# Performance work log

Hardware: AMD Instinct MI355X
Metric: run time of the kernel (lower is better)

## Reference

```python
import jax, jax.numpy as jnp
import numpy as np

HEADS = 8
DIM_HEAD = 64
SCALE = DIM_HEAD ** -0.5
EPS = 1e-7


def setup_inputs() -> dict:
    key = jax.random.key(0)
    ks = jax.random.split(key, 7)
    b, n, m, d = 8, 1024, 1024, 512
    inner = HEADS * DIM_HEAD  # 512
    s = lambda fan_in: 1.0 / np.sqrt(fan_in)
    return {
        "x": jax.random.normal(ks[0], (b, n, d), jnp.float32),
        "context": jax.random.normal(ks[1], (b, m, d), jnp.float32),
        "Wq": jax.random.normal(ks[2], (inner, d), jnp.float32) * s(d),
        "Wk": jax.random.normal(ks[3], (inner, d), jnp.float32) * s(d),
        "Wv": jax.random.normal(ks[4], (inner, d), jnp.float32) * s(d),
        "Wo": jax.random.normal(ks[5], (d, inner), jnp.float32) * s(inner),
        "bo": jnp.zeros((d,), jnp.float32),
    }


def _split_heads(t):
    # [b, n, h*d] -> [b, h, n, d]
    b, n, hd = t.shape
    return t.reshape(b, n, HEADS, DIM_HEAD).transpose(0, 2, 1, 3)


def reference(x, context, Wq, Wk, Wv, Wo, bo):
    # Linear projections (torch Linear: y = x @ W.T)
    q = _split_heads(jnp.einsum('bnd,ed->bne', x, Wq))        # [b,h,n,dh]
    k = _split_heads(jnp.einsum('bmd,ed->bme', context, Wk))  # [b,h,m,dh]
    v = _split_heads(jnp.einsum('bmd,ed->bme', context, Wv))  # [b,h,m,dh]

    sim = jnp.einsum('bhid,bhjd->bhij', q, k) * SCALE          # [b,h,n,m]

    # 'slot' attention: softmax over query dim (i), renormalize over keys (j)
    attn = jax.nn.softmax(sim, axis=2)
    attn = attn / (attn.sum(axis=-1, keepdims=True) + EPS)

    out = jnp.einsum('bhij,bhjd->bhid', attn, v)               # [b,h,n,dh]
    b, h, n, dh = out.shape
    out = out.transpose(0, 2, 1, 3).reshape(b, n, h * dh)      # [b,n,inner]
    return jnp.einsum('bne,de->bnd', out, Wo) + bo
```

## Files before the change

### kernel.cpp

```cpp
#include <hip/hip_runtime.h>

typedef __attribute__((ext_vector_type(8))) short short8;
typedef __attribute__((ext_vector_type(4))) float f32x4;
typedef __attribute__((ext_vector_type(16))) float f32x16;
typedef __attribute__((ext_vector_type(4))) unsigned short ushort4v;
typedef __attribute__((ext_vector_type(4))) unsigned int u32x4;
typedef unsigned short u16;
typedef unsigned int u32;

#define NN 1024
#define DD 512
#define DH 64
#define EXP2C 0.18033688f


__device__ __forceinline__ u16 f2bf(float f) {
    unsigned u = __float_as_uint(f);
    u += 0x7fffu + ((u >> 16) & 1u);
    return (u16)(u >> 16);
}

__device__ __forceinline__ float fexp2(float x) {
    float r;
    asm("v_exp_f32 %0, %1" : "=v"(r) : "v"(x));
    return r;
}

__device__ __forceinline__ u32 cvtpk(float a, float b) {
    u32 r;
    asm("v_cvt_pk_bf16_f32 %0, %1, %2" : "=v"(r) : "v"(a), "v"(b));
    return r;
}

__device__ __forceinline__ void stage_gll(const char* src, char* dst) {
    __builtin_amdgcn_global_load_lds(
        (const __attribute__((address_space(1))) unsigned int*)src,
        (__attribute__((address_space(3))) unsigned int*)dst, 16, 0, 0);
}

__device__ __forceinline__ short8 lds_ld128(const char* base, int row, int colbyte) {
    int off = (row * 128 + colbyte) ^ ((row & 7) << 4);
    return *(const short8*)(base + off);
}

__device__ __forceinline__ void stage128x64(const u16* g, int ldRow, char* lds,
                                            int wid, int lane) {
#pragma unroll
    for (int r = 0; r < 4; ++r) {
        int cidx = (r * 4 + wid) * 64 + lane;
        int row  = cidx >> 3;
        int ch   = (cidx & 7) ^ (row & 7);
        stage_gll((const char*)(g + row * ldRow) + ch * 16, lds + (r * 4 + wid) * 1024);
    }
}

__device__ __forceinline__ int offF2(int il, int hh, int t) {
    int c0 = t * 2 + hh;
    return ((il >> 1) << 8) + ((il & 1) << 7) + ((c0 ^ ((il >> 1) & 7)) << 4);
}

__device__ __forceinline__ int offF4(int il, int hh, int m, int tc) {
    int c0 = tc * 2 + hh;
    int line = m * 8 + (il >> 2);
    int s16 = (((il & 3) << 2) + c0) ^ ((il >> 2) & 7);
    return line * 256 + (s16 << 4);
}

__global__ void f2bf_all(const float* __restrict__ x, const float* __restrict__ ctx,
                         const float* __restrict__ Wq, const float* __restrict__ Wk,
                         const float* __restrict__ Wv, const float* __restrict__ Wo,
                         u16* __restrict__ xb, u16* __restrict__ cb,
                         u16* __restrict__ wb) {
    int i = blockIdx.x * blockDim.x + threadIdx.x;
    const float* src;
    u16* dst;
    int off;
    if (i < 1048576)      { src = x;   dst = xb; off = i; }
    else if (i < 2097152) { src = ctx; dst = cb; off = i - 1048576; }
    else {
        int wi = i - 2097152;
        int which = wi >> 16;
        off = wi & 65535;
        dst = wb + (size_t)which * 262144;
        src = (which == 0) ? Wq : (which == 1) ? Wk : (which == 2) ? Wv : Wo;
    }
    float4 v = ((const float4*)src)[off];
    ushort4v o;
    o.x = f2bf(v.x); o.y = f2bf(v.y); o.z = f2bf(v.z); o.w = f2bf(v.w);
    *(ushort4v*)(dst + (size_t)off * 4) = o;
}

__global__ __launch_bounds__(256, 2) void gemm_qkv(
    const u16* __restrict__ xb, const u16* __restrict__ cb, const u16* __restrict__ wb,
    u16* __restrict__ qb, u16* __restrict__ kb, u16* __restrict__ vT)
{
    __shared__ char As[16384];
    __shared__ char Bs[16384];
    const int z = blockIdx.z;
    const u16* A = (z == 0) ? xb : cb;
    const u16* B = wb + (size_t)z * 262144;
    const int lane = threadIdx.x & 63;
    const int wid  = threadIdx.x >> 6;
    const int wr = wid >> 1, wc = wid & 1;
    const int n = blockIdx.x + 4 * blockIdx.y;
    const int L = (n & 7) * 32 + (n >> 3);
    const int rowBase = (L >> 2) * 128;
    const int colBase = (L & 3) * 128;

    f32x4 acc[4][4] = {};
    for (int kt = 0; kt < 8; ++kt) {
        __syncthreads();
        stage128x64(A + (size_t)rowBase * DD + kt * 64, DD, As, wid, lane);
        stage128x64(B + (size_t)colBase * DD + kt * 64, DD, Bs, wid, lane);
        __syncthreads();
#pragma unroll
        for (int kk = 0; kk < 2; ++kk) {
            const int cbb = kk * 64 + (lane >> 4) * 16;
            short8 af[4], bf[4];
#pragma unroll
            for (int m = 0; m < 4; ++m) af[m] = lds_ld128(As, wr * 64 + m * 16 + (lane & 15), cbb);
#pragma unroll
            for (int q = 0; q < 4; ++q) bf[q] = lds_ld128(Bs, wc * 64 + q * 16 + (lane & 15), cbb);
#pragma unroll
            for (int m = 0; m < 4; ++m) {
#pragma unroll
                for (int q = 0; q < 4; ++q)
                    acc[m][q] = __builtin_amdgcn_mfma_f32_16x16x32_bf16(af[m], bf[q], acc[m][q], 0, 0, 0);
            }
        }
    }
#pragma unroll
    for (int m = 0; m < 4; ++m) {
#pragma unroll
        for (int q = 0; q < 4; ++q) {
            const int r0 = rowBase + wr * 64 + m * 16 + ((lane >> 4) << 2);
            const int c  = colBase + wc * 64 + q * 16 + (lane & 15);
            if (z < 2) {
                u16* O = z ? kb : qb;
#pragma unroll
                for (int g = 0; g < 4; ++g) O[(size_t)(r0 + g) * DD + c] = f2bf(acc[m][q][g]);
            } else {
                ushort4v pk;
#pragma unroll
                for (int g = 0; g < 4; ++g) pk[g] = f2bf(acc[m][q][g]);
                *(ushort4v*)(vT + (size_t)c * 8192 + r0) = pk;
            }
        }
    }
}

__global__ __launch_bounds__(256, 2) void gemm_out(
    const u16* __restrict__ A, const u16* __restrict__ B,
    float* __restrict__ Out, const float* __restrict__ bias)
{
    __shared__ char As[16384];
    __shared__ char Bs[16384];
    const int lane = threadIdx.x & 63;
    const int wid  = threadIdx.x >> 6;
    const int wr = wid >> 1, wc = wid & 1;
    const int n = blockIdx.x + 4 * blockIdx.y;
    const int L = (n & 7) * 32 + (n >> 3);
    const int rowBase = (L >> 2) * 128;
    const int colBase = (L & 3) * 128;

    f32x4 acc[4][4] = {};
    for (int kt = 0; kt < 8; ++kt) {
        __syncthreads();
        stage128x64(A + (size_t)rowBase * DD + kt * 64, DD, As, wid, lane);
        stage128x64(B + (size_t)colBase * DD + kt * 64, DD, Bs, wid, lane);
        __syncthreads();
#pragma unroll
        for (int kk = 0; kk < 2; ++kk) {
            const int cbb = kk * 64 + (lane >> 4) * 16;
            short8 af[4], bf[4];
#pragma unroll
            for (int m = 0; m < 4; ++m) af[m] = lds_ld128(As, wr * 64 + m * 16 + (lane & 15), cbb);
#pragma unroll
            for (int q = 0; q < 4; ++q) bf[q] = lds_ld128(Bs, wc * 64 + q * 16 + (lane & 15), cbb);
#pragma unroll
            for (int m = 0; m < 4; ++m) {
#pragma unroll
                for (int q = 0; q < 4; ++q)
                    acc[m][q] = __builtin_amdgcn_mfma_f32_16x16x32_bf16(af[m], bf[q], acc[m][q], 0, 0, 0);
            }
        }
    }
#pragma unroll
    for (int m = 0; m < 4; ++m) {
#pragma unroll
        for (int q = 0; q < 4; ++q) {
            const int r0 = rowBase + wr * 64 + m * 16 + ((lane >> 4) << 2);
            const int c  = colBase + wc * 64 + q * 16 + (lane & 15);
            const float bb = bias[c];
#pragma unroll
            for (int g = 0; g < 4; ++g) Out[(size_t)(r0 + g) * DD + c] = acc[m][q][g] + bb;
        }
    }
}

__global__ __launch_bounds__(256, 4) void colsum_k(
    const u16* __restrict__ qb, const u16* __restrict__ kb, float* __restrict__ lic)
{
    alignas(16) __shared__ char smem[16384];
    __shared__ float cs[128];
    const int tid = threadIdx.x;
    const int lane = tid & 63, wid = tid >> 6;
    const int il = lane & 31, hh = lane >> 5;
    const int n = blockIdx.x + 16 * blockIdx.y;
    const int L = (n & 7) * 128 + (n >> 3);
    const int jg = L & 15, bh = L >> 4;
    const int b = bh >> 3, h = bh & 7;
    const int jbp = wid & 1, ih = wid >> 1;
    const int jbase = jg * 64 + jbp * 32;

    const u16* kRow = kb + (size_t)(b * NN + jbase + il) * DD + h * DH + hh * 8;
    short8 kf[4];
#pragma unroll
    for (int t = 0; t < 4; ++t) kf[t] = *(const short8*)(kRow + t * 16);

    const int line = tid >> 4, s15 = tid & 15;
    const int slot8 = (s15 & 7) ^ (line & 7);
    const u16* qg0 = qb + (size_t)(b * NN) * DD + h * DH;
    const char* pQ0 = (const char*)(qg0 + (size_t)(line * 2 + (s15 >> 3)) * DD) + slot8 * 16;
    const char* pQ1 = pQ0 + 512 * DD * 2;
    const int dstoff = tid * 16;

    auto stageQ = [&](char* buf, const char* q0, const char* q1) {
        stage_gll(q0, buf + dstoff);
        stage_gll(q1, buf + 4096 + dstoff);
    };

    int oq[4];
#pragma unroll
    for (int t = 0; t < 4; ++t) oq[t] = offF2(il, hh, t) + ih * 4096;

    float cp[16] = {};
    stageQ(smem, pQ0, pQ1);
    pQ0 += 32768; pQ1 += 32768;
    for (int p = 0; p < 16; ++p) {
        char* buf = smem + (p & 1) * 8192;
        __syncthreads();
        if (p < 15) {
            stageQ(smem + ((p + 1) & 1) * 8192, pQ0, pQ1);
            pQ0 += 32768; pQ1 += 32768;
        }
        short8 qf[4];
#pragma unroll
        for (int t = 0; t < 4; ++t) qf[t] = *(const short8*)(buf + oq[t]);
        f32x16 sa = {};
#pragma unroll
        for (int t = 0; t < 4; ++t)
            sa = __builtin_amdgcn_mfma_f32_32x32x16_bf16(kf[t], qf[t], sa, 0, 0, 0);
#pragma unroll
        for (int r = 0; r < 16; ++r) cp[r] += fexp2(sa[r] * EXP2C);
    }
#pragma unroll
    for (int r = 0; r < 16; ++r) {
        cp[r] += __shfl_xor(cp[r], 1);
        cp[r] += __shfl_xor(cp[r], 2);
        cp[r] += __shfl_xor(cp[r], 4);
        cp[r] += __shfl_xor(cp[r], 8);
        cp[r] += __shfl_xor(cp[r], 16);
    }
    if (il == 0) {
#pragma unroll
        for (int r = 0; r < 16; ++r) cs[(jbp * 2 + ih) * 32 + hh * 16 + r] = cp[r];
    }
    __syncthreads();
    if (tid < 64) {
        int jbp2 = tid >> 5, jj = tid & 31;
        int r = (jj & 3) | ((jj >> 3) << 2);
        int h2 = (jj >> 2) & 1;
        float s = cs[(jbp2 * 2 + 0) * 32 + h2 * 16 + r] + cs[(jbp2 * 2 + 1) * 32 + h2 * 16 + r];
        lic[(size_t)bh * NN + jg * 64 + tid] = -__log2f(s);
    }
}

__global__ __launch_bounds__(256, 4) void attn_k(
    const u16* __restrict__ qb, const u16* __restrict__ kb, const u16* __restrict__ vT,
    const float* __restrict__ lic, u16* __restrict__ ob)
{
    alignas(16) __shared__ char smem[32768];
    const int tid = threadIdx.x;
    const int lane = tid & 63, wid = tid >> 6;
    const int il = lane & 31, hh = lane >> 5;
    const int n = blockIdx.x + 16 * blockIdx.y;
    const int L = (n & 7) * 128 + (n >> 3);
    const int ig = L & 15, bh = L >> 4;
    const int b = bh >> 3, h = bh & 7;
    const int ibp = wid & 1, jh = wid >> 1;
    const int ibase = ig * 64 + ibp * 32;

    const u16* qRow = qb + (size_t)(b * NN + ibase + il) * DD + h * DH + hh * 8;
    short8 qf[4];
#pragma unroll
    for (int t = 0; t < 4; ++t) qf[t] = *(const short8*)(qRow + t * 16);

    const int line = tid >> 4, s15 = tid & 15;
    const int slot8 = (s15 & 7) ^ (line & 7);
    const int s16 = s15 ^ (line & 7);
    const u16* kg0 = kb + (size_t)(b * NN) * DD + h * DH;
    const u16* vg0 = vT + (size_t)h * DH * 8192 + b * NN;
    const char* pK0 = (const char*)(kg0 + (size_t)(line * 2 + (s15 >> 3)) * DD) + slot8 * 16;
    const char* pK1 = pK0 + 512 * DD * 2;
    const char* pV0 = (const char*)(vg0 + (size_t)(line * 4 + (s16 >> 2)) * 8192) + (s16 & 3) * 16;
    const char* pV1 = pV0 + 512 * 2;
    const int dstoff = tid * 16;
    const float* licb = lic + (size_t)bh * NN + 4 * hh;

    auto stageKV = [&](char* buf, const char* k0, const char* k1,
                       const char* v0, const char* v1) {
        stage_gll(k0, buf + dstoff);
        stage_gll(k1, buf + 4096 + dstoff);
        stage_gll(v0, buf + 8192 + dstoff);
        stage_gll(v1, buf + 12288 + dstoff);
    };

    int ok[4], ov[2][2];
#pragma unroll
    for (int t = 0; t < 4; ++t) ok[t] = offF2(il, hh, t) + jh * 4096;
#pragma unroll
    for (int m = 0; m < 2; ++m)
#pragma unroll
        for (int tc = 0; tc < 2; ++tc) ov[m][tc] = offF4(il, hh, m, tc) + 8192 + jh * 4096;

    f32x16 oacc[2] = {};
    float rs = 0.0f;

    stageKV(smem, pK0, pK1, pV0, pV1);
    pK0 += 32768; pK1 += 32768; pV0 += 64; pV1 += 64;
    for (int p = 0; p < 16; ++p) {
        char* buf = smem + (p & 1) * 16384;
        __syncthreads();
        if (p < 15) {
            stageKV(smem + ((p + 1) & 1) * 16384, pK0, pK1, pV0, pV1);
            pK0 += 32768; pK1 += 32768; pV0 += 64; pV1 += 64;
        }
        const int jb = (jh * 16 + p) * 32;
        short8 kf[4];
#pragma unroll
        for (int t = 0; t < 4; ++t) kf[t] = *(const short8*)(buf + ok[t]);
        f32x16 sa = {};
#pragma unroll
        for (int t = 0; t < 4; ++t)
            sa = __builtin_amdgcn_mfma_f32_32x32x16_bf16(kf[t], qf[t], sa, 0, 0, 0);
        u32 pk[4][2];
#pragma unroll
        for (int s = 0; s < 4; ++s) {
            const float4 lc = *(const float4*)(licb + jb + 8 * s);
            const float p0 = fexp2(fmaf(sa[4 * s + 0], EXP2C, lc.x));
            const float p1 = fexp2(fmaf(sa[4 * s + 1], EXP2C, lc.y));
            const float p2 = fexp2(fmaf(sa[4 * s + 2], EXP2C, lc.z));
            const float p3 = fexp2(fmaf(sa[4 * s + 3], EXP2C, lc.w));
            rs += (p0 + p1) + (p2 + p3);
            pk[s][0] = cvtpk(p0, p1);
            pk[s][1] = cvtpk(p2, p3);
        }
        short8 vf[2][2];
#pragma unroll
        for (int m = 0; m < 2; ++m)
#pragma unroll
            for (int tc = 0; tc < 2; ++tc) vf[m][tc] = *(const short8*)(buf + ov[m][tc]);
#pragma unroll
        for (int tc = 0; tc < 2; ++tc) {
            const u32 snd0 = hh ? pk[2 * tc][0] : pk[2 * tc + 1][0];
            const u32 snd1 = hh ? pk[2 * tc][1] : pk[2 * tc + 1][1];
            const u32 rcv0 = (u32)__shfl_xor((int)snd0, 32);
            const u32 rcv1 = (u32)__shfl_xor((int)snd1, 32);
            u32x4 pw;
            pw.x = hh ? rcv0 : pk[2 * tc][0];
            pw.y = hh ? rcv1 : pk[2 * tc][1];
            pw.z = hh ? pk[2 * tc + 1][0] : rcv0;
            pw.w = hh ? pk[2 * tc + 1][1] : rcv1;
            const short8 pf = __builtin_bit_cast(short8, pw);
#pragma unroll
            for (int m = 0; m < 2; ++m)
                oacc[m] = __builtin_amdgcn_mfma_f32_32x32x16_bf16(vf[m][tc], pf, oacc[m], 0, 0, 0);
        }
    }

    rs += __shfl_xor(rs, 32);
    __syncthreads();
    float* cO = (float*)smem;
    float* cR = (float*)(smem + 16384);
    if (jh == 1) {
#pragma unroll
        for (int m = 0; m < 2; ++m)
#pragma unroll
            for (int r = 0; r < 16; ++r) cO[(ibp * 32 + m * 16 + r) * 64 + lane] = oacc[m][r];
        cR[ibp * 64 + lane] = rs;
    }
    __syncthreads();
    if (jh == 0) {
#pragma unroll
        for (int m = 0; m < 2; ++m)
#pragma unroll
            for (int r = 0; r < 16; ++r) oacc[m][r] += cO[(ibp * 32 + m * 16 + r) * 64 + lane];
        rs += cR[ibp * 64 + lane];
        const float inv = 1.0f / (rs + 1e-7f);
        u16* oRow = ob + (size_t)(b * NN + ibase + il) * DD + h * DH;
#pragma unroll
        for (int m = 0; m < 2; ++m) {
#pragma unroll
            for (int s = 0; s < 4; ++s) {
                ushort4v st;
#pragma unroll
                for (int g = 0; g < 4; ++g) st[g] = f2bf(oacc[m][4 * s + g] * inv);
                *(ushort4v*)(oRow + m * 32 + 8 * s + 4 * hh) = st;
            }
        }
    }
}


extern "C" void kernel_launch(void* const* d_in, const int* in_sizes, int n_in,
                              void* d_out, int out_size, void* d_ws, size_t ws_size,
                              hipStream_t stream)
{
    (void)in_sizes; (void)n_in; (void)out_size; (void)ws_size;
    const float* x   = (const float*)d_in[0];
    const float* ctx = (const float*)d_in[1];
    const float* Wq  = (const float*)d_in[2];
    const float* Wk  = (const float*)d_in[3];
    const float* Wv  = (const float*)d_in[4];
    const float* Wo  = (const float*)d_in[5];
    const float* bo  = (const float*)d_in[6];
    float* out = (float*)d_out;

    char* w = (char*)d_ws;
    const size_t SZBIG = 8192ull * 512 * 2;
    u16* xb  = (u16*)(w);
    u16* cb  = (u16*)(w + SZBIG);
    u16* qb  = (u16*)(w + 2 * SZBIG);
    u16* kb  = (u16*)(w + 3 * SZBIG);
    u16* vT  = (u16*)(w + 4 * SZBIG);
    u16* wb  = (u16*)(w + 5 * SZBIG);
    u16* wob = wb + 3 * 262144;
    float* lic = (float*)(w + 5 * SZBIG + 4 * 524288);
    u16* ob = xb;

    f2bf_all<<<9216, 256, 0, stream>>>(x, ctx, Wq, Wk, Wv, Wo, xb, cb, wb);

    gemm_qkv<<<dim3(4, 64, 3), 256, 0, stream>>>(xb, cb, wb, qb, kb, vT);

    colsum_k<<<dim3(16, 64), 256, 0, stream>>>(qb, kb, lic);
    attn_k  <<<dim3(16, 64), 256, 0, stream>>>(qb, kb, vT, lic, ob);

    gemm_out<<<dim3(4, 64), 256, 0, stream>>>(ob, wob, out, bo);
}
```

Before: 91.96 us.

## Triple-buffer Q/KV staging with vmcnt waits, LDS lic cache, MFMA priority

Both the colsum and attention kernels move from double to triple buffering of their staged Q or K/V tiles. They prefetch two tiles ahead, wait with explicit vmcnt counts and a single barrier per iteration, and rotate the buffer pointers. The attention kernel also copies its per-head log column sums into LDS once instead of re-reading them from global memory every iteration. s_setprio brackets the MFMA blocks to favour matrix issue. The aim is to hide global load latency and cut barrier stalls. The cost is more LDS per block (53KB in attn_k), which may reduce occupancy below the launch-bounds target.

```diff
diff --git a/kernel.cpp b/kernel.cpp
--- a/kernel.cpp
+++ b/kernel.cpp
@@ -201,7 +201,7 @@
 __global__ __launch_bounds__(256, 4) void colsum_k(
     const u16* __restrict__ qb, const u16* __restrict__ kb, float* __restrict__ lic)
 {
-    alignas(16) __shared__ char smem[16384];
+    alignas(16) __shared__ char smem[24576];
     __shared__ float cs[128];
     const int tid = threadIdx.x;
     const int lane = tid & 63, wid = tid >> 6;
@@ -234,25 +234,37 @@
 #pragma unroll
     for (int t = 0; t < 4; ++t) oq[t] = offF2(il, hh, t) + ih * 4096;
 
+    char* A0 = smem;
+    char* A1 = smem + 8192;
+    char* A2 = smem + 16384;
+
+    stageQ(A0, pQ0, pQ1); pQ0 += 32768; pQ1 += 32768;
+    stageQ(A1, pQ0, pQ1); pQ0 += 32768; pQ1 += 32768;
+    __syncthreads();
+
     float cp[16] = {};
-    stageQ(smem, pQ0, pQ1);
-    pQ0 += 32768; pQ1 += 32768;
     for (int p = 0; p < 16; ++p) {
-        char* buf = smem + (p & 1) * 8192;
-        __syncthreads();
-        if (p < 15) {
-            stageQ(smem + ((p + 1) & 1) * 8192, pQ0, pQ1);
-            pQ0 += 32768; pQ1 += 32768;
+        if (p) {
+            if (p < 15) asm volatile("s_waitcnt vmcnt(2)" ::: "memory");
+            else        asm volatile("s_waitcnt vmcnt(0)" ::: "memory");
+            __builtin_amdgcn_s_barrier();
+            asm volatile("" ::: "memory");
+        }
+        if (p + 2 < 16) {
+            stageQ(A2, pQ0, pQ1); pQ0 += 32768; pQ1 += 32768;
         }
         short8 qf[4];
 #pragma unroll
-        for (int t = 0; t < 4; ++t) qf[t] = *(const short8*)(buf + oq[t]);
+        for (int t = 0; t < 4; ++t) qf[t] = *(const short8*)(A0 + oq[t]);
         f32x16 sa = {};
+        __builtin_amdgcn_s_setprio(1);
 #pragma unroll
         for (int t = 0; t < 4; ++t)
             sa = __builtin_amdgcn_mfma_f32_32x32x16_bf16(kf[t], qf[t], sa, 0, 0, 0);
+        __builtin_amdgcn_s_setprio(0);
 #pragma unroll
         for (int r = 0; r < 16; ++r) cp[r] += fexp2(sa[r] * EXP2C);
+        char* tmp = A0; A0 = A1; A1 = A2; A2 = tmp;
     }
 #pragma unroll
     for (int r = 0; r < 16; ++r) {
@@ -280,7 +292,7 @@
     const u16* __restrict__ qb, const u16* __restrict__ kb, const u16* __restrict__ vT,
     const float* __restrict__ lic, u16* __restrict__ ob)
 {
-    alignas(16) __shared__ char smem[32768];
+    alignas(16) __shared__ char smem[53248];
     const int tid = threadIdx.x;
     const int lane = tid & 63, wid = tid >> 6;
     const int il = lane & 31, hh = lane >> 5;
@@ -290,11 +302,17 @@
     const int b = bh >> 3, h = bh & 7;
     const int ibp = wid & 1, jh = wid >> 1;
     const int ibase = ig * 64 + ibp * 32;
+    char* licLds = smem + 49152;
 
     const u16* qRow = qb + (size_t)(b * NN + ibase + il) * DD + h * DH + hh * 8;
     short8 qf[4];
 #pragma unroll
     for (int t = 0; t < 4; ++t) qf[t] = *(const short8*)(qRow + t * 16);
+
+    {
+        float4 lv = *(const float4*)(lic + (size_t)bh * NN + tid * 4);
+        *(float4*)(licLds + tid * 16) = lv;
+    }
 
     const int line = tid >> 4, s15 = tid & 15;
     const int slot8 = (s15 & 7) ^ (line & 7);
@@ -306,7 +324,6 @@
     const char* pV0 = (const char*)(vg0 + (size_t)(line * 4 + (s16 >> 2)) * 8192) + (s16 & 3) * 16;
     const char* pV1 = pV0 + 512 * 2;
     const int dstoff = tid * 16;
-    const float* licb = lic + (size_t)bh * NN + 4 * hh;
 
     auto stageKV = [&](char* buf, const char* k0, const char* k1,
                        const char* v0, const char* v1) {
@@ -324,30 +341,44 @@
 #pragma unroll
         for (int tc = 0; tc < 2; ++tc) ov[m][tc] = offF4(il, hh, m, tc) + 8192 + jh * 4096;
 
+    char* A0 = smem;
+    char* A1 = smem + 16384;
+    char* A2 = smem + 32768;
+
+    stageKV(A0, pK0, pK1, pV0, pV1);
+    pK0 += 32768; pK1 += 32768; pV0 += 64; pV1 += 64;
+    stageKV(A1, pK0, pK1, pV0, pV1);
+    pK0 += 32768; pK1 += 32768; pV0 += 64; pV1 += 64;
+    __syncthreads();
+
     f32x16 oacc[2] = {};
     float rs = 0.0f;
 
-    stageKV(smem, pK0, pK1, pV0, pV1);
-    pK0 += 32768; pK1 += 32768; pV0 += 64; pV1 += 64;
     for (int p = 0; p < 16; ++p) {
-        char* buf = smem + (p & 1) * 16384;
-        __syncthreads();
-        if (p < 15) {
-            stageKV(smem + ((p + 1) & 1) * 16384, pK0, pK1, pV0, pV1);
+        if (p) {
+            if (p < 15) asm volatile("s_waitcnt vmcnt(4)" ::: "memory");
+            else        asm volatile("s_waitcnt vmcnt(0)" ::: "memory");
+            __builtin_amdgcn_s_barrier();
+            asm volatile("" ::: "memory");
+        }
+        if (p + 2 < 16) {
+            stageKV(A2, pK0, pK1, pV0, pV1);
             pK0 += 32768; pK1 += 32768; pV0 += 64; pV1 += 64;
         }
         const int jb = (jh * 16 + p) * 32;
         short8 kf[4];
 #pragma unroll
-        for (int t = 0; t < 4; ++t) kf[t] = *(const short8*)(buf + ok[t]);
+        for (int t = 0; t < 4; ++t) kf[t] = *(const short8*)(A0 + ok[t]);
         f32x16 sa = {};
+        __builtin_amdgcn_s_setprio(1);
 #pragma unroll
         for (int t = 0; t < 4; ++t)
             sa = __builtin_amdgcn_mfma_f32_32x32x16_bf16(kf[t], qf[t], sa, 0, 0, 0);
+        __builtin_amdgcn_s_setprio(0);
         u32 pk[4][2];
 #pragma unroll
         for (int s = 0; s < 4; ++s) {
-            const float4 lc = *(const float4*)(licb + jb + 8 * s);
+            const float4 lc = *(const float4*)(licLds + (jb + 8 * s + 4 * hh) * 4);
             const float p0 = fexp2(fmaf(sa[4 * s + 0], EXP2C, lc.x));
             const float p1 = fexp2(fmaf(sa[4 * s + 1], EXP2C, lc.y));
             const float p2 = fexp2(fmaf(sa[4 * s + 2], EXP2C, lc.z));
@@ -360,7 +391,7 @@
 #pragma unroll
         for (int m = 0; m < 2; ++m)
 #pragma unroll
-            for (int tc = 0; tc < 2; ++tc) vf[m][tc] = *(const short8*)(buf + ov[m][tc]);
+            for (int tc = 0; tc < 2; ++tc) vf[m][tc] = *(const short8*)(A0 + ov[m][tc]);
 #pragma unroll
         for (int tc = 0; tc < 2; ++tc) {
             const u32 snd0 = hh ? pk[2 * tc][0] : pk[2 * tc + 1][0];
@@ -373,10 +404,13 @@
             pw.z = hh ? pk[2 * tc + 1][0] : rcv0;
             pw.w = hh ? pk[2 * tc + 1][1] : rcv1;
             const short8 pf = __builtin_bit_cast(short8, pw);
+            __builtin_amdgcn_s_setprio(1);
 #pragma unroll
             for (int m = 0; m < 2; ++m)
                 oacc[m] = __builtin_amdgcn_mfma_f32_32x32x16_bf16(vf[m][tc], pf, oacc[m], 0, 0, 0);
-        }
+            __builtin_amdgcn_s_setprio(0);
+        }
+        char* tmp = A0; A0 = A1; A1 = A2; A2 = tmp;
     }
 
     rs += __shfl_xor(rs, 32);
```

After: 96.61 us. +5.1%, slower.
